# Kernel tuning notes

Hardware: AMD Instinct MI355X
Metric: run time of the kernel (lower is better)

The kernel has to match this reference:

```python
import jax, jax.numpy as jnp
import numpy as np

B, N, C = 8, 1024, 1024
H = 16
D = C // H  # head_dim = 64


def apply_rope(t, cos, sin):
    # t: (B,H,N,D), cos/sin: (N, D//2). Interleaved-pair RoPE
    # (matches repeat_interleave(2) + stack(-y2,y1) in the torch code).
    tr = t.reshape(*t.shape[:-1], D // 2, 2)
    t1, t2 = tr[..., 0], tr[..., 1]
    o1 = t1 * cos - t2 * sin
    o2 = t2 * cos + t1 * sin
    return jnp.stack((o1, o2), axis=-1).reshape(t.shape)


def setup_inputs() -> dict:
    key = jax.random.key(0)
    k1, k2, k3, k4 = jax.random.split(key, 4)
    s = 0.02
    x = jax.random.normal(k1, (B, N, C), dtype=jnp.float32)
    w_qkv = jax.random.normal(k2, (C, 3 * C), dtype=jnp.float32) * s  # qkv_bias=False
    w_proj = jax.random.normal(k3, (C, C), dtype=jnp.float32) * s
    b_proj = jax.random.normal(k4, (C,), dtype=jnp.float32) * s
    return {"x": x, "w_qkv": w_qkv, "w_proj": w_proj, "b_proj": b_proj}


def reference(x, w_qkv, w_proj, b_proj):
    # QKV projection: (B,N,3C) -> (3,B,H,N,D)
    qkv = (x @ w_qkv).reshape(B, N, 3, H, D).transpose(2, 0, 3, 1, 4)
    q, k, v = qkv[0], qkv[1], qkv[2]

    # RoPE tables: pos = arange(N) (mask=None, no cls/registers)
    pos = jnp.arange(N, dtype=jnp.float32)
    omega = 1.0 / (10000.0 ** (jnp.arange(D // 2, dtype=jnp.float32) / (D / 2.0)))
    freq = pos[:, None] * omega  # (N, D//2)
    cos, sin = jnp.cos(freq), jnp.sin(freq)

    q = apply_rope(q, cos, sin)
    k = apply_rope(k, cos, sin)

    # Scaled dot-product attention (non-causal, no dropout in eval)
    scale = 1.0 / jnp.sqrt(jnp.float32(D))
    scores = jnp.einsum('bhqd,bhkd->bhqk', q, k) * scale
    attn = jax.nn.softmax(scores, axis=-1)
    out = jnp.einsum('bhqk,bhkd->bhqd', attn, v)

    # Merge heads + output projection
    out = out.transpose(0, 2, 1, 3).reshape(B, N, C)
    return out @ w_proj + b_proj
```

## Files before the change

kernel.cpp:

```cpp
#include <hip/hip_runtime.h>
#include <hip/hip_bf16.h>
#include <math.h>

#define Bsz  8
#define Nseq 1024
#define Cdim 1024
#define Hh   16
#define Dd   64

typedef short short8 __attribute__((ext_vector_type(8)));
typedef float floatx4 __attribute__((ext_vector_type(4)));

__device__ __forceinline__ unsigned short f2bf(float f) {
    __hip_bfloat16 h = __float2bfloat16(f);
    return __builtin_bit_cast(unsigned short, h);
}
__device__ __forceinline__ float b2f(unsigned short u) {
    return __uint_as_float(((unsigned)u) << 16);
}

__device__ __forceinline__ void async16(const void* g, void* l) {
    __builtin_amdgcn_global_load_lds(
        (const __attribute__((address_space(1))) unsigned int*)g,
        (__attribute__((address_space(3))) unsigned int*)l, 16, 0, 0);
}

__device__ __forceinline__ unsigned pack_bf16(float lo, float hi) {
    unsigned ulo = __float_as_uint(lo) + 0x8000u;
    unsigned uhi = __float_as_uint(hi) + 0x8000u;
    return __builtin_amdgcn_perm(uhi, ulo, 0x07060302);
}

__global__ __launch_bounds__(256) void rope_table(float2* __restrict__ tbl)
{
    int i = blockIdx.x * 256 + threadIdx.x;
    int n = i >> 5, p = i & 31;
    float omega = __expf(-(float)p * 0.2878231366242557f);
    float sv, cv;
    sincosf((float)n * omega, &sv, &cv);
    tbl[i] = make_float2(cv, sv);
}

__global__ __launch_bounds__(256) void convert_bf16(
    const float* __restrict__ in, unsigned short* __restrict__ out)
{
    int i = blockIdx.x * 256 + threadIdx.x;
    float4 v = ((const float4*)in)[i];
    ushort4 u;
    u.x = f2bf(v.x); u.y = f2bf(v.y); u.z = f2bf(v.z); u.w = f2bf(v.w);
    ((ushort4*)out)[i] = u;
}

__global__ __launch_bounds__(256) void transpose_bf16(
    const float* __restrict__ in, unsigned short* __restrict__ out, int R, int Ccols)
{
    __shared__ float T[64][65];
    int c0 = blockIdx.x * 64, r0 = blockIdx.y * 64;
    for (int i = threadIdx.x; i < 4096; i += 256) {
        int r = i >> 6, c = i & 63;
        T[r][c] = in[(size_t)(r0 + r) * Ccols + c0 + c];
    }
    __syncthreads();
    for (int i = threadIdx.x; i < 4096; i += 256) {
        int rr = i >> 6, cc = i & 63;
        out[(size_t)(c0 + rr) * R + r0 + cc] = f2bf(T[cc][rr]);
    }
}

__global__ __launch_bounds__(256) void rope_scatter(
    const unsigned short* __restrict__ qkv, const float2* __restrict__ rope,
    unsigned short* __restrict__ qb, unsigned short* __restrict__ kb)
{
    int i = blockIdx.x * 256 + threadIdx.x;
    int row = i >> 9;
    int col = (i & 511) * 4;
    int sec = col >> 10;
    int cc  = col & 1023;
    int h = cc >> 6, d = cc & 63;
    int b = row >> 10, n = row & 1023;

    ushort4 v = *(const ushort4*)(qkv + (size_t)row * 3072 + sec * 1024 + cc);
    float2 cs0 = rope[n * 32 + (d >> 1)];
    float2 cs1 = rope[n * 32 + (d >> 1) + 1];
    float x0 = b2f(v.x), x1 = b2f(v.y), x2 = b2f(v.z), x3 = b2f(v.w);
    float scale = (sec == 0) ? 0.125f : 1.f;
    ushort4 o;
    o.x = f2bf((x0 * cs0.x - x1 * cs0.y) * scale);
    o.y = f2bf((x1 * cs0.x + x0 * cs0.y) * scale);
    o.z = f2bf((x2 * cs1.x - x3 * cs1.y) * scale);
    o.w = f2bf((x3 * cs1.x + x2 * cs1.y) * scale);
    unsigned short* dst = (sec == 0) ? qb : kb;
    *(ushort4*)(dst + (((size_t)(b * Hh + h) * Nseq + n) * Dd + d)) = o;
}

__global__ __launch_bounds__(256) void transpose_vq(
    const unsigned short* __restrict__ qkv, unsigned short* __restrict__ out)
{
    __shared__ unsigned short T[64][68];
    const int nt = blockIdx.x, bh = blockIdx.y;
    const int b = bh >> 4, h = bh & 15;
    const int tid = threadIdx.x;

    for (int i = tid; i < 1024; i += 256) {
        int r = i >> 4, c4 = i & 15;
        const unsigned short* src =
            qkv + (size_t)(b * 1024 + nt * 64 + r) * 3072 + 2048 + h * 64;
        ushort4 v = ((const ushort4*)src)[c4];
        T[c4 * 4 + 0][r] = v.x;
        T[c4 * 4 + 1][r] = v.y;
        T[c4 * 4 + 2][r] = v.z;
        T[c4 * 4 + 3][r] = v.w;
    }
    __syncthreads();
    const size_t obase = (size_t)bh * Dd * Nseq + (size_t)nt * 64;
    for (int i = tid; i < 1024; i += 256) {
        int d = i >> 4, seg = i & 15;
        ushort4 v = *(const ushort4*)&T[d][seg * 4];
        *(ushort4*)(out + obase + (size_t)d * Nseq + seg * 4) = v;
    }
}

template <int MODE>
__global__ __launch_bounds__(256) void gemm_bf16(
    const unsigned short* __restrict__ A, const unsigned short* __restrict__ Bt,
    const float* __restrict__ bias,
    unsigned short* __restrict__ qkv, float* __restrict__ out)
{
    const int K = 1024;
    const int NW = (MODE == 0) ? 3072 : 1024;
    __shared__ short As[128][32];
    __shared__ short Bs[128][32];
    const int tid  = threadIdx.x;
    const int wave = tid >> 6, lane = tid & 63;
    const int ml = lane & 15, quad = lane >> 4;
    const int wm = wave >> 1, wn = wave & 1;
    const int bm = blockIdx.y * 128, bn = blockIdx.x * 128;

    const int gchunk = ((lane & 3) ^ ((lane >> 3) & 3)) * 8;
    const int srow   = lane >> 2;
    const int rslot  = (quad ^ ((ml >> 1) & 3)) * 8;

    floatx4 acc[4][4] = {};

    for (int k0 = 0; k0 < K; k0 += 32) {
        #pragma unroll
        for (int t = 0; t < 2; ++t) {
            int r0  = wave * 16 + t * 64;
            int row = r0 + srow;
            int kp  = k0 + gchunk;
            async16(A  + (size_t)(bm + row) * K + kp, &As[r0][0]);
            async16(Bt + (size_t)(bn + row) * K + kp, &Bs[r0][0]);
        }
        __syncthreads();

        short8 araw[4], braw[4];
        #pragma unroll
        for (int mi = 0; mi < 4; ++mi)
            araw[mi] = *(const short8*)&As[wm * 64 + mi * 16 + ml][rslot];
        #pragma unroll
        for (int ni = 0; ni < 4; ++ni)
            braw[ni] = *(const short8*)&Bs[wn * 64 + ni * 16 + ml][rslot];
        #pragma unroll
        for (int mi = 0; mi < 4; ++mi)
            #pragma unroll
            for (int ni = 0; ni < 4; ++ni)
                acc[mi][ni] = __builtin_amdgcn_mfma_f32_16x16x32_bf16(
                    araw[mi], braw[ni], acc[mi][ni], 0, 0, 0);
        __syncthreads();
    }

    if (MODE == 0) {
        #pragma unroll
        for (int ni = 0; ni < 4; ++ni) {
            int col = bn + wn * 64 + ni * 16 + ml;
            #pragma unroll
            for (int mi = 0; mi < 4; ++mi)
                #pragma unroll
                for (int r = 0; r < 4; ++r) {
                    int row = bm + wm * 64 + mi * 16 + quad * 4 + r;
                    qkv[(size_t)row * NW + col] = f2bf(acc[mi][ni][r]);
                }
        }
    } else {
        #pragma unroll
        for (int ni = 0; ni < 4; ++ni) {
            int col = bn + wn * 64 + ni * 16 + ml;
            float bv = bias[col];
            #pragma unroll
            for (int mi = 0; mi < 4; ++mi)
                #pragma unroll
                for (int r = 0; r < 4; ++r) {
                    int row = bm + wm * 64 + mi * 16 + quad * 4 + r;
                    out[(size_t)row * NW + col] = acc[mi][ni][r] + bv;
                }
        }
    }
}

__global__ __launch_bounds__(256) void attn_flash_mfma(
    const unsigned short* __restrict__ qb, const unsigned short* __restrict__ kb,
    const unsigned short* __restrict__ vt, unsigned short* __restrict__ ao)
{
    const int bh  = blockIdx.x;
    const int qt  = blockIdx.y;
    const int tid = threadIdx.x;
    const int wave = tid >> 6, lane = tid & 63;
    const int ml = lane & 15, quad = lane >> 4;
    const int lr = lane >> 3;
    const int lc = ((lane & 7) ^ lr) * 8;

    __shared__ short Qs[64][64];
    __shared__ short Ks[64][64];
    __shared__ short Vs[64][64];
    __shared__ short Ps[4][16][72];

    const size_t hbase = (size_t)bh * (Nseq * Dd);
    const int q0 = qt * 64;
    const int wq = wave * 16;

    async16(qb + hbase + (size_t)(q0 + wq + lr) * 64 + lc,     &Qs[wq][0]);
    async16(qb + hbase + (size_t)(q0 + wq + 8 + lr) * 64 + lc, &Qs[wq + 8][0]);

    float l_i = 0.f;
    floatx4 o[4] = {};

    for (int kt = 0; kt < 16; ++kt) {
        __syncthreads();
        const int k0r = kt * 64;
        async16(kb + hbase + (size_t)(k0r + wq + lr) * 64 + lc,     &Ks[wq][0]);
        async16(kb + hbase + (size_t)(k0r + wq + 8 + lr) * 64 + lc, &Ks[wq + 8][0]);
        async16(vt + ((size_t)bh * 64 + wq + lr) * Nseq + k0r + lc,     &Vs[wq][0]);
        async16(vt + ((size_t)bh * 64 + wq + 8 + lr) * Nseq + k0r + lc, &Vs[wq + 8][0]);
        __syncthreads();

        floatx4 st[4] = {};
        #pragma unroll
        for (int ks = 0; ks < 2; ++ks) {
            const int sl = ((ks * 4 + quad) ^ (ml & 7)) * 8;
            short8 qf = *(const short8*)&Qs[wq + ml][sl];
            #pragma unroll
            for (int kbk = 0; kbk < 4; ++kbk) {
                short8 kf = *(const short8*)&Ks[kbk * 16 + ml][sl];
                st[kbk] = __builtin_amdgcn_mfma_f32_16x16x32_bf16(kf, qf, st[kbk], 0, 0, 0);
            }
        }

        #pragma unroll
        for (int kbk = 0; kbk < 4; ++kbk) {
            float e0 = __expf(st[kbk][0]);
            float e1 = __expf(st[kbk][1]);
            float e2 = __expf(st[kbk][2]);
            float e3 = __expf(st[kbk][3]);
            l_i += (e0 + e1) + (e2 + e3);
            uint2 pk;
            pk.x = pack_bf16(e0, e1);
            pk.y = pack_bf16(e2, e3);
            *(uint2*)&Ps[wave][ml][kbk * 16 + quad * 4] = pk;
        }
        __syncthreads();

        #pragma unroll
        for (int ks = 0; ks < 2; ++ks) {
            const int sl = ((ks * 4 + quad) ^ (ml & 7)) * 8;
            short8 pf = *(const short8*)&Ps[wave][ml][ks * 32 + quad * 8];
            #pragma unroll
            for (int nt = 0; nt < 4; ++nt) {
                short8 vf = *(const short8*)&Vs[nt * 16 + ml][sl];
                o[nt] = __builtin_amdgcn_mfma_f32_16x16x32_bf16(pf, vf, o[nt], 0, 0, 0);
            }
        }
    }

    l_i += __shfl_xor(l_i, 16);
    l_i += __shfl_xor(l_i, 32);

    const int b = bh >> 4, h = bh & 15;
    #pragma unroll
    for (int r = 0; r < 4; ++r) {
        float lq = __shfl(l_i, quad * 4 + r);
        float inv = 1.f / lq;
        int q = q0 + wq + quad * 4 + r;
        size_t rowbase = ((size_t)(b * Nseq + q)) * Cdim + h * Dd;
        #pragma unroll
        for (int nt = 0; nt < 4; ++nt)
            ao[rowbase + nt * 16 + ml] = f2bf(o[nt][r] * inv);
    }
}

extern "C" void kernel_launch(void* const* d_in, const int* in_sizes, int n_in,
                              void* d_out, int out_size, void* d_ws, size_t ws_size,
                              hipStream_t stream) {
    const float* x      = (const float*)d_in[0];
    const float* w_qkv  = (const float*)d_in[1];
    const float* w_proj = (const float*)d_in[2];
    const float* b_proj = (const float*)d_in[3];
    float* out = (float*)d_out;

    const size_t M8 = (size_t)8 * 1024 * 1024;
    unsigned short* qb     = (unsigned short*)d_ws;
    unsigned short* kb     = qb + M8;
    unsigned short* vt     = kb + M8;
    unsigned short* xb     = vt + M8;
    unsigned short* wqkvt  = xb + M8;
    unsigned short* wprojt = wqkvt + 3 * 1024 * 1024;
    float2*         rope   = (float2*)(wprojt + 1024 * 1024);
    unsigned short* qkvws  = (unsigned short*)(rope + 32768);
    unsigned short* aob    = xb;

    rope_table<<<128, 256, 0, stream>>>(rope);
    convert_bf16<<<8192, 256, 0, stream>>>(x, xb);
    transpose_bf16<<<dim3(48, 16), 256, 0, stream>>>(w_qkv, wqkvt, 1024, 3072);
    transpose_bf16<<<dim3(16, 16), 256, 0, stream>>>(w_proj, wprojt, 1024, 1024);

    gemm_bf16<0><<<dim3(24, 64), 256, 0, stream>>>(xb, wqkvt, nullptr, qkvws, nullptr);

    rope_scatter<<<16384, 256, 0, stream>>>(qkvws, rope, qb, kb);
    transpose_vq<<<dim3(16, 128), 256, 0, stream>>>(qkvws, vt);

    attn_flash_mfma<<<dim3(128, 16), 256, 0, stream>>>(qb, kb, vt, aob);

    gemm_bf16<1><<<dim3(8, 64), 256, 0, stream>>>(aob, wprojt, b_proj, nullptr, out);
}
```

Baseline: 274.8 us.

## Double query rows per attention block to reuse K/V tiles across two query groups

Each attention block now covers 128 query rows instead of 64, and each wave handles two 16-row query groups that share every K and V fragment loaded from LDS. This halves K/V global-to-LDS traffic per query and doubles MFMA work per fragment load. The __syncthreads between writing and reading the per-wave P buffer is also dropped, since each wave only reads its own slice. In exchange the grid halves to 1024 blocks, and LDS use and register pressure (two sets of score and output accumulators) both rise, which can lower occupancy.

Measured after the change: 275.1 us. Within noise of the previous version (+0.1%).

```diff
diff --git a/kernel.cpp b/kernel.cpp
--- a/kernel.cpp
+++ b/kernel.cpp
@@ -209,81 +209,97 @@
     const int lr = lane >> 3;
     const int lc = ((lane & 7) ^ lr) * 8;
 
-    __shared__ short Qs[64][64];
+    __shared__ short Qs[128][64];
     __shared__ short Ks[64][64];
     __shared__ short Vs[64][64];
-    __shared__ short Ps[4][16][72];
+    __shared__ short Ps[4][32][72];
 
     const size_t hbase = (size_t)bh * (Nseq * Dd);
-    const int q0 = qt * 64;
-    const int wq = wave * 16;
-
-    async16(qb + hbase + (size_t)(q0 + wq + lr) * 64 + lc,     &Qs[wq][0]);
-    async16(qb + hbase + (size_t)(q0 + wq + 8 + lr) * 64 + lc, &Qs[wq + 8][0]);
-
-    float l_i = 0.f;
-    floatx4 o[4] = {};
+    const int q0 = qt * 128;
+    const int wq = wave * 32;
+    const int wk = wave * 16;
+
+    #pragma unroll
+    for (int t = 0; t < 4; ++t)
+        async16(qb + hbase + (size_t)(q0 + wq + t * 8 + lr) * 64 + lc, &Qs[wq + t * 8][0]);
+
+    float l0 = 0.f, l1 = 0.f;
+    floatx4 o[2][4] = {};
 
     for (int kt = 0; kt < 16; ++kt) {
         __syncthreads();
         const int k0r = kt * 64;
-        async16(kb + hbase + (size_t)(k0r + wq + lr) * 64 + lc,     &Ks[wq][0]);
-        async16(kb + hbase + (size_t)(k0r + wq + 8 + lr) * 64 + lc, &Ks[wq + 8][0]);
-        async16(vt + ((size_t)bh * 64 + wq + lr) * Nseq + k0r + lc,     &Vs[wq][0]);
-        async16(vt + ((size_t)bh * 64 + wq + 8 + lr) * Nseq + k0r + lc, &Vs[wq + 8][0]);
+        async16(kb + hbase + (size_t)(k0r + wk + lr) * 64 + lc,     &Ks[wk][0]);
+        async16(kb + hbase + (size_t)(k0r + wk + 8 + lr) * 64 + lc, &Ks[wk + 8][0]);
+        async16(vt + ((size_t)bh * 64 + wk + lr) * Nseq + k0r + lc,     &Vs[wk][0]);
+        async16(vt + ((size_t)bh * 64 + wk + 8 + lr) * Nseq + k0r + lc, &Vs[wk + 8][0]);
         __syncthreads();
 
-        floatx4 st[4] = {};
+        floatx4 st[2][4] = {};
         #pragma unroll
         for (int ks = 0; ks < 2; ++ks) {
             const int sl = ((ks * 4 + quad) ^ (ml & 7)) * 8;
-            short8 qf = *(const short8*)&Qs[wq + ml][sl];
+            short8 qf0 = *(const short8*)&Qs[wq + ml][sl];
+            short8 qf1 = *(const short8*)&Qs[wq + 16 + ml][sl];
             #pragma unroll
             for (int kbk = 0; kbk < 4; ++kbk) {
                 short8 kf = *(const short8*)&Ks[kbk * 16 + ml][sl];
-                st[kbk] = __builtin_amdgcn_mfma_f32_16x16x32_bf16(kf, qf, st[kbk], 0, 0, 0);
+                st[0][kbk] = __builtin_amdgcn_mfma_f32_16x16x32_bf16(kf, qf0, st[0][kbk], 0, 0, 0);
+                st[1][kbk] = __builtin_amdgcn_mfma_f32_16x16x32_bf16(kf, qf1, st[1][kbk], 0, 0, 0);
             }
         }
 
         #pragma unroll
-        for (int kbk = 0; kbk < 4; ++kbk) {
-            float e0 = __expf(st[kbk][0]);
-            float e1 = __expf(st[kbk][1]);
-            float e2 = __expf(st[kbk][2]);
-            float e3 = __expf(st[kbk][3]);
-            l_i += (e0 + e1) + (e2 + e3);
-            uint2 pk;
-            pk.x = pack_bf16(e0, e1);
-            pk.y = pack_bf16(e2, e3);
-            *(uint2*)&Ps[wave][ml][kbk * 16 + quad * 4] = pk;
-        }
-        __syncthreads();
+        for (int qg = 0; qg < 2; ++qg) {
+            float lacc = 0.f;
+            #pragma unroll
+            for (int kbk = 0; kbk < 4; ++kbk) {
+                float e0 = __expf(st[qg][kbk][0]);
+                float e1 = __expf(st[qg][kbk][1]);
+                float e2 = __expf(st[qg][kbk][2]);
+                float e3 = __expf(st[qg][kbk][3]);
+                lacc += (e0 + e1) + (e2 + e3);
+                uint2 pk;
+                pk.x = pack_bf16(e0, e1);
+                pk.y = pack_bf16(e2, e3);
+                *(uint2*)&Ps[wave][qg * 16 + ml][kbk * 16 + quad * 4] = pk;
+            }
+            if (qg == 0) l0 += lacc; else l1 += lacc;
+        }
 
         #pragma unroll
         for (int ks = 0; ks < 2; ++ks) {
             const int sl = ((ks * 4 + quad) ^ (ml & 7)) * 8;
-            short8 pf = *(const short8*)&Ps[wave][ml][ks * 32 + quad * 8];
+            short8 pf0 = *(const short8*)&Ps[wave][ml][ks * 32 + quad * 8];
+            short8 pf1 = *(const short8*)&Ps[wave][16 + ml][ks * 32 + quad * 8];
             #pragma unroll
             for (int nt = 0; nt < 4; ++nt) {
                 short8 vf = *(const short8*)&Vs[nt * 16 + ml][sl];
-                o[nt] = __builtin_amdgcn_mfma_f32_16x16x32_bf16(pf, vf, o[nt], 0, 0, 0);
+                o[0][nt] = __builtin_amdgcn_mfma_f32_16x16x32_bf16(pf0, vf, o[0][nt], 0, 0, 0);
+                o[1][nt] = __builtin_amdgcn_mfma_f32_16x16x32_bf16(pf1, vf, o[1][nt], 0, 0, 0);
             }
         }
     }
 
-    l_i += __shfl_xor(l_i, 16);
-    l_i += __shfl_xor(l_i, 32);
+    l0 += __shfl_xor(l0, 16);
+    l0 += __shfl_xor(l0, 32);
+    l1 += __shfl_xor(l1, 16);
+    l1 += __shfl_xor(l1, 32);
 
     const int b = bh >> 4, h = bh & 15;
     #pragma unroll
-    for (int r = 0; r < 4; ++r) {
-        float lq = __shfl(l_i, quad * 4 + r);
-        float inv = 1.f / lq;
-        int q = q0 + wq + quad * 4 + r;
-        size_t rowbase = ((size_t)(b * Nseq + q)) * Cdim + h * Dd;
-        #pragma unroll
-        for (int nt = 0; nt < 4; ++nt)
-            ao[rowbase + nt * 16 + ml] = f2bf(o[nt][r] * inv);
+    for (int qg = 0; qg < 2; ++qg) {
+        float lsrc = (qg == 0) ? l0 : l1;
+        #pragma unroll
+        for (int r = 0; r < 4; ++r) {
+            float lq = __shfl(lsrc, quad * 4 + r);
+            float inv = 1.f / lq;
+            int q = q0 + wq + qg * 16 + quad * 4 + r;
+            size_t rowbase = ((size_t)(b * Nseq + q)) * Cdim + h * Dd;
+            #pragma unroll
+            for (int nt = 0; nt < 4; ++nt)
+                ao[rowbase + nt * 16 + ml] = f2bf(o[qg][nt][r] * inv);
+        }
     }
 }
 
@@ -317,7 +333,7 @@
     rope_scatter<<<16384, 256, 0, stream>>>(qkvws, rope, qb, kb);
     transpose_vq<<<dim3(16, 128), 256, 0, stream>>>(qkvws, vt);
 
-    attn_flash_mfma<<<dim3(128, 16), 256, 0, stream>>>(qb, kb, vt, aob);
+    attn_flash_mfma<<<dim3(128, 8), 256, 0, stream>>>(qb, kb, vt, aob);
 
     gemm_bf16<1><<<dim3(8, 64), 256, 0, stream>>>(aob, wprojt, b_proj, nullptr, out);
 }
```
